# Kernel tuning notes

Measured on AMD Instinct MI355X. Metric: run time of the kernel, lower is better.

The kernel has to match this reference:

```python
import jax, jax.numpy as jnp
import numpy as np

D_MODEL = 2048
NUM_HEADS = 16
NUM_KV_HEADS = 4
HEAD_DIM = D_MODEL // NUM_HEADS  # 128
B, T = 2, 2048


def setup_inputs() -> dict:
    key = jax.random.key(0)
    ks = jax.random.split(key, 9)
    d_kv = NUM_KV_HEADS * HEAD_DIM
    s = 1.0 / np.sqrt(D_MODEL)
    return {
        "x": jax.random.normal(ks[0], (B, T, D_MODEL), dtype=jnp.float32),
        "Wq": jax.random.normal(ks[1], (D_MODEL, D_MODEL), dtype=jnp.float32) * s,
        "bq": jnp.zeros((D_MODEL,), dtype=jnp.float32),
        "Wk": jax.random.normal(ks[2], (D_MODEL, d_kv), dtype=jnp.float32) * s,
        "bk": jnp.zeros((d_kv,), dtype=jnp.float32),
        "Wv": jax.random.normal(ks[3], (D_MODEL, d_kv), dtype=jnp.float32) * s,
        "bv": jnp.zeros((d_kv,), dtype=jnp.float32),
        "Wo": jax.random.normal(ks[4], (D_MODEL, D_MODEL), dtype=jnp.float32) * s,
        "bo": jnp.zeros((D_MODEL,), dtype=jnp.float32),
    }


def reference(x, Wq, bq, Wk, bk, Wv, bv, Wo, bo):
    b, t, _ = x.shape
    # projections
    q = x @ Wq + bq                      # [B,T,D]
    k = x @ Wk + bk                      # [B,T,KVH*Dh]
    v = x @ Wv + bv
    q = q.reshape(b, t, NUM_HEADS, HEAD_DIM)      # [B,T,H,Dh]
    k = k.reshape(b, t, NUM_KV_HEADS, HEAD_DIM)   # [B,T,KVH,Dh]
    v = v.reshape(b, t, NUM_KV_HEADS, HEAD_DIM)
    repeat = NUM_HEADS // NUM_KV_HEADS
    k = jnp.repeat(k, repeat, axis=2)              # [B,T,H,Dh]
    v = jnp.repeat(v, repeat, axis=2)
    scores = jnp.einsum('bthd,bshd->bhts', q, k) / jnp.sqrt(
        jnp.asarray(HEAD_DIM, dtype=x.dtype))
    mask = jnp.tril(jnp.ones((t, t), dtype=x.dtype))
    # faithful to source: multiplicative mask plus large negative on masked
    scores = scores * mask - 1e10 * (1.0 - mask)
    probs = jax.nn.softmax(scores, axis=-1)        # [B,H,T,S]
    out = jnp.einsum('bhts,bshd->bthd', probs, v)  # [B,T,H,Dh]
    out = out.reshape(b, t, NUM_HEADS * HEAD_DIM)  # merge heads
    return out @ Wo + bo                           # [B,T,D]
```

## Files before the change

### kernel.cpp

```cpp
#include <hip/hip_runtime.h>

typedef __attribute__((ext_vector_type(8))) __bf16 bf16x8;
typedef __attribute__((ext_vector_type(4))) float f32x4;
typedef __attribute__((ext_vector_type(4))) short short4v;

#define MFMA16(a,b,c)  __builtin_amdgcn_mfma_f32_16x16x32_bf16((a),(b),(c),0,0,0)
#define MFMA16K(a,b,c) __builtin_amdgcn_mfma_f32_16x16x16bf16_1k((a),(b),(c),0,0,0)

__device__ __forceinline__ short f2bf(float f){
  union { float f; unsigned u; } x; x.f = f;
  return (short)((x.u + 0x7fffu + ((x.u >> 16) & 1u)) >> 16);
}
__device__ __forceinline__ unsigned bits(float f){
  union { float f; unsigned u; } x; x.f = f; return x.u;
}

__device__ __forceinline__ void gld16(void* lds, const void* g){
  __builtin_amdgcn_global_load_lds(
      (const __attribute__((address_space(1))) unsigned*)g,
      (__attribute__((address_space(3))) unsigned*)lds, 16, 0, 0);
}


__global__ __launch_bounds__(256) void k_cvt8(const float* __restrict__ x,
                                              short* __restrict__ xb){
  long i = (long)blockIdx.x * 256 + threadIdx.x;
  const float4* xv = (const float4*)x;
  float4 a = xv[2*i], c = xv[2*i+1];
  short s[8] = {f2bf(a.x),f2bf(a.y),f2bf(a.z),f2bf(a.w),
                f2bf(c.x),f2bf(c.y),f2bf(c.z),f2bf(c.w)};
  *(uint4*)&xb[8*i] = *(uint4*)s;
}

__global__ void k_wt(const float* __restrict__ W, short* __restrict__ Wt, int N){
  __shared__ float tile[32][33];
  int tx = threadIdx.x, ty = threadIdx.y;
  int k0 = blockIdx.y*32, n0 = blockIdx.x*32;
  for (int j=0;j<32;j+=8)
    tile[ty+j][tx] = W[(size_t)(k0+ty+j)*N + n0 + tx];
  __syncthreads();
  for (int j=0;j<32;j+=8)
    Wt[(size_t)(n0+ty+j)*2048 + k0 + tx] = f2bf(tile[tx][ty+j]);
}

__global__ void k_bias(const float* __restrict__ bq, const float* __restrict__ bk,
                       const float* __restrict__ bv, float* __restrict__ outb){
  int i = blockIdx.x*256 + threadIdx.x;
  float v = (i < 2048) ? bq[i] : (i < 2560 ? bk[i-2048] : bv[i-2560]);
  outb[i] = v;
}

__global__ void k_vt(const short* __restrict__ qkv, short* __restrict__ Vt){
  __shared__ short tile[32][33];
  int tx = threadIdx.x, ty = threadIdx.y;
  int t0 = blockIdx.x*32, c0 = blockIdx.y*32;
  for (int j=0;j<32;j+=8)
    tile[ty+j][tx] = qkv[(size_t)(t0+ty+j)*3072 + 2560 + c0 + tx];
  __syncthreads();
  int b = t0 >> 11, t_in_b = t0 & 2047;
  for (int j=0;j<32;j+=8){
    int col = c0 + ty + j;
    int kvh = col >> 7, d = col & 127;
    Vt[((size_t)((b*4 + kvh)*128 + d))*2048 + t_in_b + tx] = tile[tx][ty+j];
  }
}

template<int OUT_BF16>
__global__ __launch_bounds__(256) void gemm_bt(const short* __restrict__ A,
    const short* __restrict__ Bt, const float* __restrict__ bias,
    void* __restrict__ Cv, int M, int N, int K){
  __shared__ short As[128*32];
  __shared__ short Bs[128*32];
  const int tid = threadIdx.x;
  const int w = tid >> 6, lane = tid & 63, l15 = lane & 15, quad = lane >> 4;
  const int wr = w >> 1, wc = w & 1;
  const int m0 = blockIdx.y*128, n0 = blockIdx.x*128;
  const int lrow = lane >> 2, lcol = (lane & 3)*8;
  const short* Ag = A  + (size_t)(m0 + w*32 + lrow)*K + lcol;
  const short* Bg = Bt + (size_t)(n0 + w*32 + lrow)*K + lcol;
  short* AsW0 = &As[(w*32)*32];
  short* AsW1 = &As[(w*32+16)*32];
  short* BsW0 = &Bs[(w*32)*32];
  short* BsW1 = &Bs[(w*32+16)*32];
  const size_t r16K = (size_t)16*K;
  f32x4 acc[4][4] = {};
  for (int kt = 0; kt < K; kt += 32){
    gld16(AsW0, Ag + kt);
    gld16(AsW1, Ag + kt + r16K);
    gld16(BsW0, Bg + kt);
    gld16(BsW1, Bg + kt + r16K);
    __syncthreads();
    bf16x8 af[4], bfr[4];
#pragma unroll
    for (int i=0;i<4;i++){
      af[i]  = *(const bf16x8*)&As[(wr*64 + i*16 + l15)*32 + quad*8];
      bfr[i] = *(const bf16x8*)&Bs[(wc*64 + i*16 + l15)*32 + quad*8];
    }
#pragma unroll
    for (int mi=0;mi<4;mi++)
#pragma unroll
      for (int nj=0;nj<4;nj++)
        acc[mi][nj] = MFMA16(af[mi], bfr[nj], acc[mi][nj]);
    __syncthreads();
  }
  float bv[4];
#pragma unroll
  for (int nj=0;nj<4;nj++) bv[nj] = bias[n0 + wc*64 + nj*16 + l15];
#pragma unroll
  for (int mi=0;mi<4;mi++){
    int row = m0 + wr*64 + mi*16 + quad*4;
#pragma unroll
    for (int nj=0;nj<4;nj++){
      int col = n0 + wc*64 + nj*16 + l15;
#pragma unroll
      for (int r=0;r<4;r++){
        float v = acc[mi][nj][r] + bv[nj];
        if (OUT_BF16) ((short*)Cv)[(size_t)(row+r)*N + col] = f2bf(v);
        else          ((float*)Cv)[(size_t)(row+r)*N + col] = v;
      }
    }
  }
}

__global__ __launch_bounds__(128) void k_attn(const short* __restrict__ qkv,
                                              const short* __restrict__ Vt,
                                              short* __restrict__ attn){
  constexpr float COEF = 0.12752365f;
  __shared__ short SM[16384];
  const int tid = threadIdx.x, w = tid >> 6, lane = tid & 63;
  const int l15 = lane & 15, quad = lane >> 4;
  const int p = blockIdx.x, h = blockIdx.y, b = blockIdx.z, kvh = h >> 2;

  const short* kb[4];
  const short* vb[4];
#pragma unroll
  for (int j=0;j<4;j++){
    int rK = w*16 + j*4 + (lane >> 4);
    int cK = (lane & 15) ^ (rK & 15);
    kb[j] = qkv + (size_t)(b*2048 + rK)*3072 + 2048 + kvh*128 + cK*8;
    int dV = w*64 + j*16 + (lane >> 2);
    int cV = (lane & 3) ^ (dV & 3);
    vb[j] = Vt + ((size_t)((b*4 + kvh)*128 + dV))*2048 + cV*8;
  }
  short* KdstBase0 = &SM[0       + w*256*8];
  short* VdstBase0 = &SM[4096    + w*256*8];

  int buf = 0;
#pragma unroll
  for (int j=0;j<4;j++){
    gld16(KdstBase0 + j*512, kb[j]);
    gld16(VdstBase0 + j*512, vb[j]);
  }

  for (int sp = 0; sp < 2; sp++){
    const int qi = sp ? (31 - p) : p;
    const int qw = qi*64 + w*32;
    bf16x8 qf[2][4];
    {
      const short* qbase = qkv + ((size_t)(b*2048 + qw + l15))*3072 + h*128 + quad*8;
#pragma unroll
      for (int qs=0;qs<2;qs++)
#pragma unroll
        for (int d4=0;d4<4;d4++)
          qf[qs][d4] = *(const bf16x8*)(qbase + (size_t)qs*16*3072 + d4*32);
    }
    f32x4 accO[2][8] = {};
    float lsum[2] = {0.f, 0.f};
    const int nst = 2*qi + 2;

    for (int st = 0; st < nst; st++){
      __syncthreads();
      const int cur = buf;
      const int nb = buf ^ 1;
      {
        int nxt = -1;
        if (st + 1 < nst) nxt = (st + 1) * 32;
        else if (sp == 0) nxt = 0;
        if (nxt >= 0){
          short* Kd = &SM[nb*8192 + w*256*8];
          short* Vd = &SM[nb*8192 + 4096 + w*256*8];
          const size_t ko = (size_t)nxt * 3072;
#pragma unroll
          for (int j=0;j<4;j++){
            gld16(Kd + j*512, kb[j] + ko);
            gld16(Vd + j*512, vb[j] + nxt);
          }
        }
      }
      const int s0 = st * 32;
      if (s0 <= qw + 31){
        const short* Kb = &SM[cur*8192];
        const short* Vb = &SM[cur*8192 + 4096];
        bf16x8 kf[2][4];
#pragma unroll
        for (int ss=0;ss<2;ss++)
#pragma unroll
          for (int d4=0;d4<4;d4++){
            int slot = (ss*16 + l15)*16 + ((d4*4 + quad) ^ l15);
            kf[ss][d4] = *(const bf16x8*)&Kb[slot*8];
          }
        short4v pf[2][2];
#pragma unroll
        for (int qs=0;qs<2;qs++){
          f32x4 sa[2] = {};
#pragma unroll
          for (int d4=0;d4<4;d4++){
            sa[0] = MFMA16(kf[0][d4], qf[qs][d4], sa[0]);
            sa[1] = MFMA16(kf[1][d4], qf[qs][d4], sa[1]);
          }
          const int qmin = qw + qs*16;
          const bool mneed = (s0 + 31 > qmin);
          const int qgl = qmin + l15;
#pragma unroll
          for (int sub=0;sub<2;sub++){
            float pr[4];
#pragma unroll
            for (int r=0;r<4;r++){
              float e = __builtin_amdgcn_exp2f(sa[sub][r] * COEF);
              int sg = s0 + sub*16 + quad*4 + r;
              if (mneed && (sg > qgl)) e = 0.f;
              pr[r] = e;
            }
            lsum[qs] += (pr[0]+pr[1]) + (pr[2]+pr[3]);
            union { unsigned u[2]; short4v s; } pk;
            pk.u[0] = __builtin_amdgcn_perm(bits(pr[1]), bits(pr[0]), 0x07060302u);
            pk.u[1] = __builtin_amdgcn_perm(bits(pr[3]), bits(pr[2]), 0x07060302u);
            pf[qs][sub] = pk.s;
          }
        }
#pragma unroll
        for (int sub=0;sub<2;sub++)
#pragma unroll
          for (int dt=0;dt<8;dt++){
            int slot = (dt*16 + l15)*4 + ((sub*2 + (quad>>1)) ^ (l15 & 3));
            short4v vf = *(const short4v*)&Vb[slot*8 + (quad&1)*4];
            accO[0][dt] = MFMA16K(vf, pf[0][sub], accO[0][dt]);
            accO[1][dt] = MFMA16K(vf, pf[1][sub], accO[1][dt]);
          }
      }
      buf = nb;
    }
#pragma unroll
    for (int qs=0;qs<2;qs++){
      float s = lsum[qs];
      s += __shfl_xor(s, 16);
      s += __shfl_xor(s, 32);
      float inv = 1.0f / s;
      short* obase = attn + ((size_t)(b*2048 + qw + qs*16 + l15))*2048
                   + h*128 + quad*4;
#pragma unroll
      for (int dt=0;dt<8;dt++){
        float o0 = accO[qs][dt][0]*inv, o1 = accO[qs][dt][1]*inv;
        float o2 = accO[qs][dt][2]*inv, o3 = accO[qs][dt][3]*inv;
        union { unsigned u[2]; short4v s; } ok;
        ok.u[0] = __builtin_amdgcn_perm(bits(o1), bits(o0), 0x07060302u);
        ok.u[1] = __builtin_amdgcn_perm(bits(o3), bits(o2), 0x07060302u);
        *(short4v*)(obase + dt*16) = ok.s;
      }
    }
  }
}

extern "C" void kernel_launch(void* const* d_in, const int* in_sizes, int n_in,
                              void* d_out, int out_size, void* d_ws, size_t ws_size,
                              hipStream_t stream){
  const float* x  = (const float*)d_in[0];
  const float* Wq = (const float*)d_in[1];
  const float* bq = (const float*)d_in[2];
  const float* Wk = (const float*)d_in[3];
  const float* bk = (const float*)d_in[4];
  const float* Wv = (const float*)d_in[5];
  const float* bv = (const float*)d_in[6];
  const float* Wo = (const float*)d_in[7];
  const float* bo = (const float*)d_in[8];
  float* out = (float*)d_out;
  char* ws = (char*)d_ws;

  short* xb    = (short*)(ws + 0);
  short* WtQKV = (short*)(ws + (size_t)16*1024*1024);
  short* WoT   = (short*)(ws + (size_t)28*1024*1024);
  float* biasQ = (float*)(ws + (size_t)36*1024*1024);
  short* qkv   = (short*)(ws + (size_t)37*1024*1024);
  short* Vt    = (short*)(ws + (size_t)61*1024*1024);
  short* attn  = (short*)(ws + 0);

  k_cvt8<<<4096, 256, 0, stream>>>(x, xb);
  k_wt<<<dim3(64,64), dim3(32,8), 0, stream>>>(Wq, WtQKV, 2048);
  k_wt<<<dim3(16,64), dim3(32,8), 0, stream>>>(Wk, WtQKV + (size_t)2048*2048, 512);
  k_wt<<<dim3(16,64), dim3(32,8), 0, stream>>>(Wv, WtQKV + (size_t)2560*2048, 512);
  k_wt<<<dim3(64,64), dim3(32,8), 0, stream>>>(Wo, WoT, 2048);
  k_bias<<<12, 256, 0, stream>>>(bq, bk, bv, biasQ);
  gemm_bt<1><<<dim3(24,32), 256, 0, stream>>>(xb, WtQKV, biasQ, qkv, 4096, 3072, 2048);
  k_vt<<<dim3(128,16), dim3(32,8), 0, stream>>>(qkv, Vt);
  k_attn<<<dim3(16,16,2), 128, 0, stream>>>(qkv, Vt, attn);
  gemm_bt<0><<<dim3(16,32), 256, 0, stream>>>(attn, WoT, bo, out, 4096, 2048, 2048);
}
```

Before: 351.6 us.

## Split attention block across four waves with 16 query rows each

The attention kernel now launches 256 threads (4 waves) per block, each wave handling 16 query rows instead of 32, and the K/V tile loads are divided across four waves. The V LDS swizzle gains an extra XOR term to reduce bank conflicts. This halves per-wave accumulator registers and adds latency hiding through more waves. In exchange each wave reloads K fragments for fewer queries, so LDS read traffic per MFMA increases.

```diff
diff --git a/kernel.cpp b/kernel.cpp
--- a/kernel.cpp
+++ b/kernel.cpp
@@ -122,7 +122,7 @@
   }
 }
 
-__global__ __launch_bounds__(128) void k_attn(const short* __restrict__ qkv,
+__global__ __launch_bounds__(256) void k_attn(const short* __restrict__ qkv,
                                               const short* __restrict__ Vt,
                                               short* __restrict__ attn){
   constexpr float COEF = 0.12752365f;
@@ -131,41 +131,39 @@
   const int l15 = lane & 15, quad = lane >> 4;
   const int p = blockIdx.x, h = blockIdx.y, b = blockIdx.z, kvh = h >> 2;
 
-  const short* kb[4];
-  const short* vb[4];
-#pragma unroll
-  for (int j=0;j<4;j++){
-    int rK = w*16 + j*4 + (lane >> 4);
+  const short* kb[2];
+  const short* vb[2];
+#pragma unroll
+  for (int j=0;j<2;j++){
+    int rK = w*8 + j*4 + (lane >> 4);
     int cK = (lane & 15) ^ (rK & 15);
     kb[j] = qkv + (size_t)(b*2048 + rK)*3072 + 2048 + kvh*128 + cK*8;
-    int dV = w*64 + j*16 + (lane >> 2);
-    int cV = (lane & 3) ^ (dV & 3);
+    int dV = w*32 + j*16 + (lane >> 2);
+    int cV = (lane & 3) ^ (dV & 3) ^ ((dV >> 2) & 3);
     vb[j] = Vt + ((size_t)((b*4 + kvh)*128 + dV))*2048 + cV*8;
   }
-  short* KdstBase0 = &SM[0       + w*256*8];
-  short* VdstBase0 = &SM[4096    + w*256*8];
+  short* K0 = &SM[w*1024];
+  short* V0 = &SM[4096 + w*1024];
 
   int buf = 0;
 #pragma unroll
-  for (int j=0;j<4;j++){
-    gld16(KdstBase0 + j*512, kb[j]);
-    gld16(VdstBase0 + j*512, vb[j]);
+  for (int j=0;j<2;j++){
+    gld16(K0 + j*512, kb[j]);
+    gld16(V0 + j*512, vb[j]);
   }
 
   for (int sp = 0; sp < 2; sp++){
     const int qi = sp ? (31 - p) : p;
-    const int qw = qi*64 + w*32;
-    bf16x8 qf[2][4];
+    const int qw = qi*64 + w*16;
+    bf16x8 qf[4];
     {
       const short* qbase = qkv + ((size_t)(b*2048 + qw + l15))*3072 + h*128 + quad*8;
 #pragma unroll
-      for (int qs=0;qs<2;qs++)
-#pragma unroll
-        for (int d4=0;d4<4;d4++)
-          qf[qs][d4] = *(const bf16x8*)(qbase + (size_t)qs*16*3072 + d4*32);
-    }
-    f32x4 accO[2][8] = {};
-    float lsum[2] = {0.f, 0.f};
+      for (int d4=0;d4<4;d4++)
+        qf[d4] = *(const bf16x8*)(qbase + d4*32);
+    }
+    f32x4 accO[8] = {};
+    float lsum = 0.f;
     const int nst = 2*qi + 2;
 
     for (int st = 0; st < nst; st++){
@@ -177,18 +175,18 @@
         if (st + 1 < nst) nxt = (st + 1) * 32;
         else if (sp == 0) nxt = 0;
         if (nxt >= 0){
-          short* Kd = &SM[nb*8192 + w*256*8];
-          short* Vd = &SM[nb*8192 + 4096 + w*256*8];
+          short* Kd = &SM[nb*8192 + w*1024];
+          short* Vd = &SM[nb*8192 + 4096 + w*1024];
           const size_t ko = (size_t)nxt * 3072;
 #pragma unroll
-          for (int j=0;j<4;j++){
+          for (int j=0;j<2;j++){
             gld16(Kd + j*512, kb[j] + ko);
             gld16(Vd + j*512, vb[j] + nxt);
           }
         }
       }
       const int s0 = st * 32;
-      if (s0 <= qw + 31){
+      if (s0 <= qw + 15){
         const short* Kb = &SM[cur*8192];
         const short* Vb = &SM[cur*8192 + 4096];
         bf16x8 kf[2][4];
@@ -199,59 +197,53 @@
             int slot = (ss*16 + l15)*16 + ((d4*4 + quad) ^ l15);
             kf[ss][d4] = *(const bf16x8*)&Kb[slot*8];
           }
-        short4v pf[2][2];
-#pragma unroll
-        for (int qs=0;qs<2;qs++){
-          f32x4 sa[2] = {};
-#pragma unroll
-          for (int d4=0;d4<4;d4++){
-            sa[0] = MFMA16(kf[0][d4], qf[qs][d4], sa[0]);
-            sa[1] = MFMA16(kf[1][d4], qf[qs][d4], sa[1]);
-          }
-          const int qmin = qw + qs*16;
-          const bool mneed = (s0 + 31 > qmin);
-          const int qgl = qmin + l15;
-#pragma unroll
-          for (int sub=0;sub<2;sub++){
-            float pr[4];
-#pragma unroll
-            for (int r=0;r<4;r++){
-              float e = __builtin_amdgcn_exp2f(sa[sub][r] * COEF);
-              int sg = s0 + sub*16 + quad*4 + r;
-              if (mneed && (sg > qgl)) e = 0.f;
-              pr[r] = e;
-            }
-            lsum[qs] += (pr[0]+pr[1]) + (pr[2]+pr[3]);
-            union { unsigned u[2]; short4v s; } pk;
-            pk.u[0] = __builtin_amdgcn_perm(bits(pr[1]), bits(pr[0]), 0x07060302u);
-            pk.u[1] = __builtin_amdgcn_perm(bits(pr[3]), bits(pr[2]), 0x07060302u);
-            pf[qs][sub] = pk.s;
-          }
+        f32x4 sa[2] = {};
+#pragma unroll
+        for (int d4=0;d4<4;d4++){
+          sa[0] = MFMA16(kf[0][d4], qf[d4], sa[0]);
+          sa[1] = MFMA16(kf[1][d4], qf[d4], sa[1]);
         }
+        short4v pf[2];
+        const bool mneed = (s0 + 31 > qw);
+        const int qgl = qw + l15;
+#pragma unroll
+        for (int sub=0;sub<2;sub++){
+          float pr[4];
+#pragma unroll
+          for (int r=0;r<4;r++){
+            float e = __builtin_amdgcn_exp2f(sa[sub][r] * COEF);
+            int sg = s0 + sub*16 + quad*4 + r;
+            if (mneed && (sg > qgl)) e = 0.f;
+            pr[r] = e;
+          }
+          lsum += (pr[0]+pr[1]) + (pr[2]+pr[3]);
+          union { unsigned u[2]; short4v s; } pk;
+          pk.u[0] = __builtin_amdgcn_perm(bits(pr[1]), bits(pr[0]), 0x07060302u);
+          pk.u[1] = __builtin_amdgcn_perm(bits(pr[3]), bits(pr[2]), 0x07060302u);
+          pf[sub] = pk.s;
+        }
 #pragma unroll
         for (int sub=0;sub<2;sub++)
 #pragma unroll
           for (int dt=0;dt<8;dt++){
-            int slot = (dt*16 + l15)*4 + ((sub*2 + (quad>>1)) ^ (l15 & 3));
+            int slot = (dt*16 + l15)*4 +
+                       ((sub*2 + (quad>>1)) ^ (l15 & 3) ^ ((l15 >> 2) & 3));
             short4v vf = *(const short4v*)&Vb[slot*8 + (quad&1)*4];
-            accO[0][dt] = MFMA16K(vf, pf[0][sub], accO[0][dt]);
-            accO[1][dt] = MFMA16K(vf, pf[1][sub], accO[1][dt]);
+            accO[dt] = MFMA16K(vf, pf[sub], accO[dt]);
           }
       }
       buf = nb;
     }
-#pragma unroll
-    for (int qs=0;qs<2;qs++){
-      float s = lsum[qs];
+    {
+      float s = lsum;
       s += __shfl_xor(s, 16);
       s += __shfl_xor(s, 32);
       float inv = 1.0f / s;
-      short* obase = attn + ((size_t)(b*2048 + qw + qs*16 + l15))*2048
-                   + h*128 + quad*4;
+      short* obase = attn + ((size_t)(b*2048 + qw + l15))*2048 + h*128 + quad*4;
 #pragma unroll
       for (int dt=0;dt<8;dt++){
-        float o0 = accO[qs][dt][0]*inv, o1 = accO[qs][dt][1]*inv;
-        float o2 = accO[qs][dt][2]*inv, o3 = accO[qs][dt][3]*inv;
+        float o0 = accO[dt][0]*inv, o1 = accO[dt][1]*inv;
+        float o2 = accO[dt][2]*inv, o3 = accO[dt][3]*inv;
         union { unsigned u[2]; short4v s; } ok;
         ok.u[0] = __builtin_amdgcn_perm(bits(o1), bits(o0), 0x07060302u);
         ok.u[1] = __builtin_amdgcn_perm(bits(o3), bits(o2), 0x07060302u);
@@ -292,6 +284,6 @@
   k_bias<<<12, 256, 0, stream>>>(bq, bk, bv, biasQ);
   gemm_bt<1><<<dim3(24,32), 256, 0, stream>>>(xb, WtQKV, biasQ, qkv, 4096, 3072, 2048);
   k_vt<<<dim3(128,16), dim3(32,8), 0, stream>>>(qkv, Vt);
-  k_attn<<<dim3(16,16,2), 128, 0, stream>>>(qkv, Vt, attn);
+  k_attn<<<dim3(16,16,2), 256, 0, stream>>>(qkv, Vt, attn);
   gemm_bt<0><<<dim3(16,32), 256, 0, stream>>>(attn, WoT, bo, out, 4096, 2048, 2048);
 }
```

Result: faster. 332.0 us (-5.6%).
